# Kernel tuning notes

Measured on AMD Instinct MI355X. Metric: run time of the kernel, lower is better.

## Reference

```python
import jax, jax.numpy as jnp
import numpy as np

B, T, M_DIM, P_DIM = 32, 192, 256, 16
D, HE, HD, HG = 1024, 1024, 1024, 512
NH, DH, DFF, NL = 16, 64, 4096, 8
CTX = 10
E = P_DIM // 2  # num_experts = d_phase // 2
PRELU_A = 0.25  # torch PReLU default init slope (treated as constant)
LN_EPS = 1e-5


def prelu(x):
    return jnp.where(x >= 0, x, PRELU_A * x)


def layer_norm(x, g, b):
    m = x.mean(-1, keepdims=True)
    v = ((x - m) ** 2).mean(-1, keepdims=True)
    return (x - m) * jax.lax.rsqrt(v + LN_EPS) * g + b


def setup_inputs() -> dict:
    key = jax.random.key(0)
    ks = iter(jax.random.split(key, 64))
    w = lambda *s: jax.random.normal(next(ks), s, jnp.float32) * 0.02
    return dict(
        motion=jax.random.normal(next(ks), (B, T, M_DIM), jnp.float32),
        phase=jax.random.normal(next(ks), (B, T, P_DIM), jnp.float32),
        enc_W1=w(M_DIM + 1 + P_DIM, HE), enc_b1=w(HE), enc_W2=w(HE, D), enc_b2=w(D),
        kf_W1=w(2, D), kf_b1=w(D), kf_W2=w(D, D), kf_b2=w(D),
        rp_W1=w(1, DH), rp_b1=w(DH), rp_W2=w(DH, DH), rp_b2=w(DH),
        att_Wq=w(NL, D, NH * DH), att_bq=w(NL, NH * DH),
        att_Wk=w(NL, D, NH * DH), att_bk=w(NL, NH * DH),
        att_Wv=w(NL, D, NH * DH), att_bv=w(NL, NH * DH),
        att_Wo=w(NL, NH * DH, D), att_bo=w(NL, D),
        att_ln_g=jnp.ones((NL, D)), att_ln_b=jnp.zeros((NL, D)),
        pff_W1=w(NL, D, DFF), pff_b1=w(NL, DFF),
        pff_W2=w(NL, DFF, D), pff_b2=w(NL, D),
        pff_ln_g=jnp.ones((NL, D)), pff_ln_b=jnp.zeros((NL, D)),
        fin_ln_g=jnp.ones(D), fin_ln_b=jnp.zeros(D),
        pd_W1=w(D, HD), pd_b1=w(HD), pd_W2=w(HD, P_DIM), pd_b2=w(P_DIM),
        g_W1=w(P_DIM, HG), g_b1=w(HG), g_W2=w(HG, HG), g_b2=w(HG),
        g_W3=w(HG, E), g_b3=w(E),
        md_W0=w(E, D, HD), md_b0=w(E, HD),
        md_W1=w(E, HD, HD), md_b1=w(E, HD),
        md_W2=w(E, HD, M_DIM), md_b2=w(E, M_DIM),
    )


def reference(motion, phase, enc_W1, enc_b1, enc_W2, enc_b2,
              kf_W1, kf_b1, kf_W2, kf_b2, rp_W1, rp_b1, rp_W2, rp_b2,
              att_Wq, att_bq, att_Wk, att_bk, att_Wv, att_bv, att_Wo, att_bo,
              att_ln_g, att_ln_b, pff_W1, pff_b1, pff_W2, pff_b2, pff_ln_g, pff_ln_b,
              fin_ln_g, fin_ln_b, pd_W1, pd_b1, pd_W2, pd_b2,
              g_W1, g_b1, g_W2, g_b2, g_W3, g_b3,
              md_W0, md_b0, md_W1, md_b1, md_W2, md_b2):
    frames = jnp.arange(T)
    # eval mode: no midway targets; keyframes = context frames + last frame
    key_mask = (frames < CTX) | (frames == T - 1)          # [T]
    dm = key_mask.astype(motion.dtype)[:, None]            # data mask [T,1]
    x = jnp.concatenate([motion * dm,
                         jnp.broadcast_to(dm, (B, T, 1)),
                         phase * dm], axis=-1)
    x = prelu(x @ enc_W1 + enc_b1)
    x = prelu(x @ enc_W2 + enc_b2)                          # [B,T,D]
    # keyframe position embedding (distance to last context / target frame)
    ctx_idx = (frames - (CTX - 1)).astype(x.dtype)
    tgt_idx = -(frames - (T - 1)).astype(x.dtype)
    kp = jnp.stack([ctx_idx, tgt_idx], axis=-1)            # [T,2]
    x = x + (prelu(kp @ kf_W1 + kf_b1) @ kf_W2 + kf_b2)
    # relative position embedding, offsets -(T-1)..(T-1)
    rp = jnp.arange(-T + 1, T, dtype=x.dtype)[:, None]     # [2T-1,1]
    rel = prelu(rp @ rp_W1 + rp_b1) @ rp_W2 + rp_b2        # [2T-1,DH]
    rel_idx = frames[None, :] - frames[:, None] + (T - 1)  # [T,T] -> index into 2T-1
    blocked = ~key_mask                                    # attention mask: only attend to keyframes
    neg = jnp.asarray(-1e9, x.dtype)
    scale = 1.0 / np.sqrt(DH)

    def block(x, p):
        Wq, bq, Wk, bk, Wv, bv, Wo, bo, lg, lb, pW1, pb1, pW2, pb2, plg, plb = p
        h = layer_norm(x, lg, lb)                          # pre_lnorm
        q = (h @ Wq + bq).reshape(B, T, NH, DH)
        k = (h @ Wk + bk).reshape(B, T, NH, DH)
        v = (h @ Wv + bv).reshape(B, T, NH, DH)
        ac = jnp.einsum('bind,bjnd->bnij', q, k)           # content score
        bd = jnp.einsum('bind,rd->bnir', q, rel)           # rel-pos score (shared across heads' rel emb)
        bd = jnp.take_along_axis(bd, jnp.broadcast_to(rel_idx[None, None], ac.shape), axis=-1)
        s = (ac + bd) * scale
        s = jnp.where(blocked[None, None, None, :], neg, s)
        a = jax.nn.softmax(s, axis=-1)
        o = jnp.einsum('bnij,bjnd->bind', a, v).reshape(B, T, NH * DH)
        x = x + o @ Wo + bo
        h2 = layer_norm(x, plg, plb)
        x = x + jax.nn.relu(h2 @ pW1 + pb1) @ pW2 + pb2    # positionwise FF
        return x, None

    layer_params = (att_Wq, att_bq, att_Wk, att_bk, att_Wv, att_bv, att_Wo, att_bo,
                    att_ln_g, att_ln_b, pff_W1, pff_b1, pff_W2, pff_b2, pff_ln_g, pff_ln_b)
    x, _ = jax.lax.scan(block, x, layer_params)
    x = layer_norm(x, fin_ln_g, fin_ln_b)                  # final LN (pre_lnorm)
    # phase decoder
    phase_out = prelu(x @ pd_W1 + pd_b1) @ pd_W2 + pd_b2   # [B,T,P]
    # gating network -> per-frame soft expert weights
    h = prelu(phase_out @ g_W1 + g_b1)
    h = prelu(h @ g_W2 + g_b2)
    gate = jax.nn.softmax(h @ g_W3 + g_b3, axis=-1)        # [B,T,E]

    def mlin(y, W, b):
        # MultiLinear + per-frame expert blend: sum_e gate_e * (y @ W_e + b_e)
        return jnp.einsum('btd,edh,bte->bth', y, W, gate) + jnp.einsum('bte,eh->bth', gate, b)

    y = prelu(mlin(x, md_W0, md_b0))
    y = prelu(mlin(y, md_W1, md_b1))
    y = mlin(y, md_W2, md_b2)                              # [B,T,M]
    return y, phase_out
```

## Files before the change

### kernel.cpp

```cpp
#include <hip/hip_runtime.h>
#include <stdint.h>

typedef unsigned short u16;
typedef __attribute__((ext_vector_type(4))) float f32x4;
typedef __attribute__((ext_vector_type(8))) __bf16 bf16x8;

#define NT 6144
#define TT 192
#define PRELU_A 0.25f

__device__ __forceinline__ u16 f2bf(float f) {
  unsigned u = __float_as_uint(f);
  u += 0x7fffu + ((u >> 16) & 1u);
  return (u16)(u >> 16);
}
__device__ __forceinline__ float bf2f(u16 u) {
  return __uint_as_float(((unsigned)u) << 16);
}

__device__ __forceinline__ void gload16(const u16* g, __bf16* l) {
  auto* l3 = reinterpret_cast<__attribute__((address_space(3))) __bf16*>(
      reinterpret_cast<uintptr_t>(l));
  const auto* g1 = reinterpret_cast<const __attribute__((address_space(1))) u16*>(
      reinterpret_cast<uintptr_t>(g));
  __builtin_amdgcn_global_load_lds(g1, l3, 16, 0, 0);
}

__global__ __launch_bounds__(256)
void transpose_bf16(const float* __restrict__ src, u16* __restrict__ dst,
                    int K, int N, int Kp, int Np, long sstride, long dstride)
{
  src += (long)blockIdx.z * sstride;
  dst += (long)blockIdx.z * dstride;
  __shared__ float tile[64][65];
  const int kt = blockIdx.y * 64, nt = blockIdx.x * 64;
  #pragma unroll
  for (int i = 0; i < 16; ++i) {
    int idx = threadIdx.x + i*256;
    int kl = idx >> 6, nl = idx & 63;
    int k = kt + kl, n = nt + nl;
    tile[kl][nl] = (k < K && n < N) ? src[(long)k*N + n] : 0.f;
  }
  __syncthreads();
  #pragma unroll
  for (int i = 0; i < 16; ++i) {
    int idx = threadIdx.x + i*256;
    int nl = idx >> 6, kl = idx & 63;
    int n = nt + nl, k = kt + kl;
    if (n < Np && k < Kp) dst[(long)n*Kp + k] = f2bf(tile[kl][nl]);
  }
}

template<int MR, int HM>
__device__ __forceinline__ void epilogue_store(
    f32x4 (&acc)[MR][4], long arow0, long brow0, int wm, int wn, int lane,
    const float* bias, int biasN,
    float* Cf, int ldc, int Nf, int accum,
    u16* Cb, int ldcb, int Nb, int act)
{
  const int rbase = wm*HM + ((lane >> 4) << 2);
  const int cbase = wn*64 + (lane & 15);
  #pragma unroll
  for (int m = 0; m < MR; ++m) {
    #pragma unroll
    for (int n = 0; n < 4; ++n) {
      const long gcol = brow0 + cbase + n*16;
      const float bv = (bias && gcol < biasN) ? bias[gcol] : 0.f;
      #pragma unroll
      for (int r = 0; r < 4; ++r) {
        const long grow = arow0 + rbase + m*16 + r;
        float v = acc[m][n][r] + bv;
        if (act == 1) v = fmaxf(v, 0.f);
        else if (act == 2) v = (v >= 0.f) ? v : PRELU_A * v;
        if (Cf && gcol < Nf) {
          const long idx = grow * (long)ldc + gcol;
          Cf[idx] = accum ? (Cf[idx] + v) : v;
        }
        if (Cb && gcol < Nb) Cb[grow * (long)ldcb + gcol] = f2bf(v);
      }
    }
  }
}

__global__ __launch_bounds__(256, 3)
void gemm64(const u16* __restrict__ A, const u16* __restrict__ Bt,
            const float* __restrict__ bias, int biasN,
            float* __restrict__ Cf, int ldc, int Nf, int accum,
            u16* __restrict__ Cb, int ldcb, int Nb,
            int K, int act)
{
  __shared__ __bf16 As[2*64*64];
  __shared__ __bf16 Bs[2*128*64];
  const int tid = threadIdx.x;
  const int wid = tid >> 6;
  const int lane = tid & 63;
  const int wm = wid >> 1, wn = wid & 1;
  const long arow0 = (long)blockIdx.x * 64;
  const long brow0 = (long)blockIdx.y * 128;
  const int lr  = lane >> 3;
  const int lko = ((lane & 7) ^ (lane >> 3)) << 3;

  f32x4 acc[2][4];
  #pragma unroll
  for (int m = 0; m < 2; ++m)
    #pragma unroll
    for (int n = 0; n < 4; ++n) acc[m][n] = (f32x4)0.f;

  const int aro = lane & 15;
  const int g = lane >> 4;

  auto stage = [&](int buf, int kt) {
    #pragma unroll
    for (int c = wid; c < 24; c += 4) {
      if (c < 8) gload16(A + (arow0 + c*8 + lr)*K + kt + lko, As + buf*(64*64) + c*512);
      else       gload16(Bt + (brow0 + (c-8)*8 + lr)*K + kt + lko,
                         Bs + buf*(128*64) + (c-8)*512);
    }
  };

  const int nt = K >> 6;
  stage(0, 0);
  for (int t = 0; t < nt; ++t) {
    if (t + 1 < nt) {
      stage((t+1) & 1, (t+1) << 6);
      asm volatile("s_waitcnt vmcnt(6)" ::: "memory");
    } else {
      asm volatile("s_waitcnt vmcnt(0)" ::: "memory");
    }
    __builtin_amdgcn_s_barrier();
    __builtin_amdgcn_sched_barrier(0);
    const __bf16* Ab = As + (t&1)*(64*64);
    const __bf16* Bb = Bs + (t&1)*(128*64);
    #pragma unroll
    for (int kk = 0; kk < 2; ++kk) {
      bf16x8 af[2], bfv[4];
      #pragma unroll
      for (int m = 0; m < 2; ++m) {
        const int R = wm*32 + m*16 + aro;
        af[m] = *(const bf16x8*)(Ab + R*64 + (((kk*4 + g) ^ (R & 7)) << 3));
      }
      #pragma unroll
      for (int n = 0; n < 4; ++n) {
        const int R = wn*64 + n*16 + aro;
        bfv[n] = *(const bf16x8*)(Bb + R*64 + (((kk*4 + g) ^ (R & 7)) << 3));
      }
      #pragma unroll
      for (int m = 0; m < 2; ++m)
        #pragma unroll
        for (int n = 0; n < 4; ++n)
          acc[m][n] = __builtin_amdgcn_mfma_f32_16x16x32_bf16(af[m], bfv[n], acc[m][n], 0, 0, 0);
    }
    __builtin_amdgcn_sched_barrier(0);
    __builtin_amdgcn_s_barrier();
  }
  epilogue_store<2,32>(acc, arow0, brow0, wm, wn, lane,
                       bias, biasN, Cf, ldc, Nf, accum, Cb, ldcb, Nb, act);
}

__global__ __launch_bounds__(256, 3)
void gemm128(const u16* __restrict__ A, const u16* __restrict__ Bt,
             const float* __restrict__ bias, int biasN,
             float* __restrict__ Cf, int ldc, int Nf, int accum,
             u16* __restrict__ Cb, int ldcb, int Nb,
             int K, int act)
{
  __shared__ __bf16 As[3*128*32];
  __shared__ __bf16 Bs[3*128*32];
  const int tid = threadIdx.x;
  const int wid = tid >> 6;
  const int lane = tid & 63;
  const int wm = wid >> 1, wn = wid & 1;
  const long arow0 = (long)blockIdx.x * 128;
  const long brow0 = (long)blockIdx.y * 128;
  const int srow = lane >> 2;
  const int skoff = ((lane & 3) ^ ((lane >> 3) & 3)) << 3;

  f32x4 acc[4][4];
  #pragma unroll
  for (int m = 0; m < 4; ++m)
    #pragma unroll
    for (int n = 0; n < 4; ++n) acc[m][n] = (f32x4)0.f;

  const int aro = lane & 15;
  const int g = lane >> 4;

  auto stage = [&](int buf, int kt) {
    #pragma unroll
    for (int c = wid; c < 16; c += 4) {
      if (c < 8) gload16(A + (arow0 + c*16 + srow)*K + kt + skoff, As + buf*4096 + c*512);
      else       gload16(Bt + (brow0 + (c-8)*16 + srow)*K + kt + skoff,
                         Bs + buf*4096 + (c-8)*512);
    }
  };

  const int nt = K >> 5;
  stage(0, 0);
  if (nt > 1) stage(1, 32);

  int bcur = 0;
  for (int t = 0; t < nt; ++t) {
    if (t + 1 < nt) asm volatile("s_waitcnt vmcnt(4)" ::: "memory");
    else            asm volatile("s_waitcnt vmcnt(0)" ::: "memory");
    __builtin_amdgcn_s_barrier();
    __builtin_amdgcn_sched_barrier(0);
    if (t + 2 < nt) {
      int bnext = bcur + 2; if (bnext >= 3) bnext -= 3;
      stage(bnext, (t + 2) * 32);
    }
    const __bf16* Ab = As + bcur*4096;
    const __bf16* Bb = Bs + bcur*4096;
    bf16x8 af[4], bfv[4];
    #pragma unroll
    for (int m = 0; m < 4; ++m) {
      const int R = wm*64 + m*16 + aro;
      af[m] = *(const bf16x8*)(Ab + R*32 + ((g ^ ((R >> 1) & 3)) << 3));
    }
    #pragma unroll
    for (int n = 0; n < 4; ++n) {
      const int R = wn*64 + n*16 + aro;
      bfv[n] = *(const bf16x8*)(Bb + R*32 + ((g ^ ((R >> 1) & 3)) << 3));
    }
    #pragma unroll
    for (int m = 0; m < 4; ++m)
      #pragma unroll
      for (int n = 0; n < 4; ++n)
        acc[m][n] = __builtin_amdgcn_mfma_f32_16x16x32_bf16(af[m], bfv[n], acc[m][n], 0, 0, 0);
    __builtin_amdgcn_sched_barrier(0);
    bcur = (bcur + 1 == 3) ? 0 : bcur + 1;
  }
  epilogue_store<4,64>(acc, arow0, brow0, wm, wn, lane,
                       bias, biasN, Cf, ldc, Nf, accum, Cb, ldcb, Nb, act);
}

__global__ __launch_bounds__(256)
void moe_blend(const u16* __restrict__ C, const float* __restrict__ gate,
               int e0, int nE, int H, float* __restrict__ acc, int init,
               int act, u16* __restrict__ outb, float* __restrict__ outf)
{
  const int h4 = H >> 2;
  const long idx = (long)blockIdx.x*256 + threadIdx.x;
  if (idx >= (long)NT * h4) return;
  const long t = idx / h4;
  const int h = (int)(idx % h4) << 2;
  const long rowW = (long)nE * H;
  float4 s;
  if (init) { s.x = s.y = s.z = s.w = 0.f; }
  else s = ((const float4*)acc)[idx];
  for (int j = 0; j < nE; ++j) {
    const float gv = gate[t*8 + e0 + j];
    const ushort4 c4 = *(const ushort4*)(C + t*rowW + j*H + h);
    s.x += gv * bf2f(c4.x); s.y += gv * bf2f(c4.y);
    s.z += gv * bf2f(c4.z); s.w += gv * bf2f(c4.w);
  }
  const bool fin = (outb != nullptr) || (outf != nullptr);
  if (!fin) { ((float4*)acc)[idx] = s; return; }
  if (act == 2) {
    s.x = (s.x >= 0.f) ? s.x : PRELU_A * s.x;
    s.y = (s.y >= 0.f) ? s.y : PRELU_A * s.y;
    s.z = (s.z >= 0.f) ? s.z : PRELU_A * s.z;
    s.w = (s.w >= 0.f) ? s.w : PRELU_A * s.w;
  }
  if (outf) ((float4*)outf)[idx] = s;
  if (outb) {
    ushort4 o; o.x = f2bf(s.x); o.y = f2bf(s.y); o.z = f2bf(s.z); o.w = f2bf(s.w);
    *(ushort4*)(outb + t*(long)H + h) = o;
  }
}

__global__ __launch_bounds__(256)
void build_xin(const float* __restrict__ motion, const float* __restrict__ phase,
               u16* __restrict__ xin)
{
  const long idx = (long)blockIdx.x*256 + threadIdx.x;
  if (idx >= (long)NT*320) return;
  const int c = (int)(idx % 320);
  const long row = idx / 320;
  const int t = (int)(row % TT);
  const bool dm = (t < 10) || (t == TT-1);
  float v;
  if (c < 256)       v = dm ? motion[row*256 + c] : 0.f;
  else if (c == 256) v = dm ? 1.f : 0.f;
  else if (c < 273)  v = dm ? phase[row*16 + (c-257)] : 0.f;
  else               v = 0.f;
  xin[idx] = f2bf(v);
}

__global__ __launch_bounds__(256)
void build_kp(u16* __restrict__ kp)
{
  const int idx = blockIdx.x*256 + threadIdx.x;
  if (idx >= 256*64) return;
  const int r = idx / 64, c = idx % 64;
  float v = 0.f;
  if (r < TT) {
    if (c == 0) v = (float)(r - 9);
    else if (c == 1) v = (float)(TT-1 - r);
  }
  kp[idx] = f2bf(v);
}

__global__ __launch_bounds__(256)
void cat_kv_bias(const float* __restrict__ bk, const float* __restrict__ bv,
                 float* __restrict__ kvb)
{
  const int idx = blockIdx.x*256 + threadIdx.x;
  if (idx >= 8*2048) return;
  const int l = idx >> 11, c = idx & 2047;
  kvb[idx] = (c < 1024) ? bk[l*1024 + c] : bv[l*1024 + c - 1024];
}

__global__ __launch_bounds__(64)
void relpos(const float* __restrict__ W1, const float* __restrict__ b1,
            const float* __restrict__ W2, const float* __restrict__ b2,
            float* __restrict__ rel)
{
  const int r = blockIdx.x;
  const int d = threadIdx.x;
  __shared__ float h[64];
  const float rp = (float)(r - (TT-1));
  float hv = rp * W1[d] + b1[d];
  hv = (hv >= 0.f) ? hv : PRELU_A * hv;
  h[d] = hv;
  __syncthreads();
  if (r < 2*TT - 1) {
    float o = b2[d];
    for (int j = 0; j < 64; ++j) o += h[j] * W2[j*64 + d];
    rel[r*64 + d] = o;
  } else {
    rel[r*64 + d] = 0.f;
  }
}

__global__ __launch_bounds__(256)
void ln_bf16(const float* __restrict__ x, const float* __restrict__ g,
             const float* __restrict__ b, u16* __restrict__ out)
{
  const long row = blockIdx.x;
  const float4 v = ((const float4*)(x + row*1024))[threadIdx.x];
  float s  = v.x + v.y + v.z + v.w;
  float s2 = v.x*v.x + v.y*v.y + v.z*v.z + v.w*v.w;
  #pragma unroll
  for (int m = 32; m; m >>= 1) { s += __shfl_xor(s, m); s2 += __shfl_xor(s2, m); }
  __shared__ float red[8];
  const int wid = threadIdx.x >> 6;
  if ((threadIdx.x & 63) == 0) { red[wid] = s; red[wid+4] = s2; }
  __syncthreads();
  s  = red[0] + red[1] + red[2] + red[3];
  s2 = red[4] + red[5] + red[6] + red[7];
  const float mean = s * (1.f/1024.f);
  const float var  = fmaxf(s2 * (1.f/1024.f) - mean*mean, 0.f);
  const float rs   = rsqrtf(var + 1e-5f);
  const float4 gg = ((const float4*)g)[threadIdx.x];
  const float4 bb = ((const float4*)b)[threadIdx.x];
  ushort4 o;
  o.x = f2bf((v.x-mean)*rs*gg.x + bb.x);
  o.y = f2bf((v.y-mean)*rs*gg.y + bb.y);
  o.z = f2bf((v.z-mean)*rs*gg.z + bb.z);
  o.w = f2bf((v.w-mean)*rs*gg.w + bb.w);
  ((ushort4*)(out + row*1024))[threadIdx.x] = o;
}

__global__ __launch_bounds__(128)
void gather_hk(const u16* __restrict__ h, u16* __restrict__ hk)
{
  const int r = blockIdx.x;
  uint4 val;
  if (r < 352) {
    const int b = r / 11, j = r - b*11;
    const int fr = (j < 10) ? j : (TT-1);
    val = ((const uint4*)(h + (long)(b*TT + fr)*1024))[threadIdx.x];
  } else { val.x = val.y = val.z = val.w = 0u; }
  ((uint4*)(hk + (long)r*1024))[threadIdx.x] = val;
}

__global__ __launch_bounds__(256)
void attn11(const float* __restrict__ q, const float* __restrict__ kv,
            const float* __restrict__ rel, u16* __restrict__ o)
{
  const int w = (blockIdx.x << 2) + (threadIdx.x >> 6);
  const int lane = threadIdx.x & 63;
  const int n = w & 15;
  const int row = w >> 4;
  const int b = row / TT, i = row - b*TT;
  const float qd = q[(long)row*1024 + n*64 + lane];
  float s[11];
  #pragma unroll
  for (int j = 0; j < 11; ++j) {
    const int kf = (j < 10) ? j : (TT-1);
    float t = qd * (kv[(long)(b*11 + j)*2048 + n*64 + lane]
                    + rel[(kf - i + TT-1)*64 + lane]);
    #pragma unroll
    for (int m = 32; m; m >>= 1) t += __shfl_xor(t, m);
    s[j] = t * 0.125f;
  }
  float mx = s[0];
  #pragma unroll
  for (int j = 1; j < 11; ++j) mx = fmaxf(mx, s[j]);
  float den = 0.f, e[11];
  #pragma unroll
  for (int j = 0; j < 11; ++j) { e[j] = __expf(s[j] - mx); den += e[j]; }
  const float inv = 1.f / den;
  float od = 0.f;
  #pragma unroll
  for (int j = 0; j < 11; ++j)
    od += e[j] * kv[(long)(b*11 + j)*2048 + 1024 + n*64 + lane];
  o[(long)row*1024 + n*64 + lane] = f2bf(od * inv);
}

__global__ __launch_bounds__(256)
void kfadd(float* __restrict__ x, const float* __restrict__ kfe)
{
  const long idx = (long)blockIdx.x*256 + threadIdx.x;
  if (idx >= (long)NT*256) return;
  const int t = (int)((idx >> 8) % TT);
  const int c4 = (int)(idx & 255);
  float4 a = ((float4*)x)[idx];
  const float4 kk = ((const float4*)kfe)[t*256 + c4];
  a.x += kk.x; a.y += kk.y; a.z += kk.z; a.w += kk.w;
  ((float4*)x)[idx] = a;
}

__global__ __launch_bounds__(256)
void softmax8(const float* __restrict__ lg, float* __restrict__ gate)
{
  const int t = blockIdx.x*256 + threadIdx.x;
  if (t >= NT) return;
  float v[8], mx = -1e30f;
  #pragma unroll
  for (int e = 0; e < 8; ++e) { v[e] = lg[t*8 + e]; mx = fmaxf(mx, v[e]); }
  float den = 0.f;
  #pragma unroll
  for (int e = 0; e < 8; ++e) { v[e] = __expf(v[e] - mx); den += v[e]; }
  const float inv = 1.f / den;
  #pragma unroll
  for (int e = 0; e < 8; ++e) gate[t*8 + e] = v[e] * inv;
}

extern "C" void kernel_launch(void* const* d_in, const int* in_sizes, int n_in,
                              void* d_out, int out_size, void* d_ws, size_t ws_size,
                              hipStream_t stream)
{
  (void)in_sizes; (void)n_in; (void)out_size; (void)ws_size;
  const float* motion  = (const float*)d_in[0];
  const float* phase   = (const float*)d_in[1];
  const float* enc_W1  = (const float*)d_in[2];
  const float* enc_b1  = (const float*)d_in[3];
  const float* enc_W2  = (const float*)d_in[4];
  const float* enc_b2  = (const float*)d_in[5];
  const float* kf_W1   = (const float*)d_in[6];
  const float* kf_b1   = (const float*)d_in[7];
  const float* kf_W2   = (const float*)d_in[8];
  const float* kf_b2   = (const float*)d_in[9];
  const float* rp_W1   = (const float*)d_in[10];
  const float* rp_b1   = (const float*)d_in[11];
  const float* rp_W2   = (const float*)d_in[12];
  const float* rp_b2   = (const float*)d_in[13];
  const float* att_Wq  = (const float*)d_in[14];
  const float* att_bq  = (const float*)d_in[15];
  const float* att_Wk  = (const float*)d_in[16];
  const float* att_bk  = (const float*)d_in[17];
  const float* att_Wv  = (const float*)d_in[18];
  const float* att_bv  = (const float*)d_in[19];
  const float* att_Wo  = (const float*)d_in[20];
  const float* att_bo  = (const float*)d_in[21];
  const float* att_ln_g = (const float*)d_in[22];
  const float* att_ln_b = (const float*)d_in[23];
  const float* pff_W1  = (const float*)d_in[24];
  const float* pff_b1  = (const float*)d_in[25];
  const float* pff_W2  = (const float*)d_in[26];
  const float* pff_b2  = (const float*)d_in[27];
  const float* pff_ln_g = (const float*)d_in[28];
  const float* pff_ln_b = (const float*)d_in[29];
  const float* fin_ln_g = (const float*)d_in[30];
  const float* fin_ln_b = (const float*)d_in[31];
  const float* pd_W1   = (const float*)d_in[32];
  const float* pd_b1   = (const float*)d_in[33];
  const float* pd_W2   = (const float*)d_in[34];
  const float* pd_b2   = (const float*)d_in[35];
  const float* g_W1    = (const float*)d_in[36];
  const float* g_b1    = (const float*)d_in[37];
  const float* g_W2    = (const float*)d_in[38];
  const float* g_b2    = (const float*)d_in[39];
  const float* g_W3    = (const float*)d_in[40];
  const float* g_b3    = (const float*)d_in[41];
  const float* md_W0   = (const float*)d_in[42];
  const float* md_b0   = (const float*)d_in[43];
  const float* md_W1   = (const float*)d_in[44];
  const float* md_b1   = (const float*)d_in[45];
  const float* md_W2   = (const float*)d_in[46];
  const float* md_b2   = (const float*)d_in[47];

  char* wsp = (char*)d_ws;
  size_t off = 0;
  auto alloc = [&](size_t bytes) -> char* {
    char* p = wsp + off;
    off += (bytes + 255) & ~(size_t)255;
    return p;
  };

  u16* encW1T = (u16*)alloc((size_t)1024*320*2);
  u16* encW2T = (u16*)alloc((size_t)1024*1024*2);
  u16* kfW1T  = (u16*)alloc((size_t)1024*64*2);
  u16* kfW2T  = (u16*)alloc((size_t)1024*1024*2);
  u16* WqT    = (u16*)alloc((size_t)8*1024*1024*2);
  u16* kvT    = (u16*)alloc((size_t)8*2048*1024*2);
  u16* WoT    = (u16*)alloc((size_t)8*1024*1024*2);
  u16* F1T    = (u16*)alloc((size_t)8*4096*1024*2);
  u16* F2T    = (u16*)alloc((size_t)8*1024*4096*2);
  u16* pdW1T  = (u16*)alloc((size_t)1024*1024*2);
  u16* pdW2T  = (u16*)alloc((size_t)128*1024*2);
  u16* gW1T   = (u16*)alloc((size_t)512*64*2);
  u16* gW2T   = (u16*)alloc((size_t)512*512*2);
  u16* gW3T   = (u16*)alloc((size_t)128*512*2);
  u16* md0T   = (u16*)alloc((size_t)8*1024*1024*2);
  u16* md1T   = (u16*)alloc((size_t)8*1024*1024*2);
  u16* md2T   = (u16*)alloc((size_t)8*256*1024*2);

  float* x    = (float*)alloc((size_t)NT*1024*4);
  float* rel  = (float*)alloc((size_t)384*64*4);
  u16*   kp   = (u16*)  alloc((size_t)256*64*2);
  u16*   kf1  = (u16*)  alloc((size_t)256*1024*2);
  float* kfe  = (float*)alloc((size_t)256*1024*4);
  u16*   hk   = (u16*)  alloc((size_t)384*1024*2);
  float* kvb  = (float*)alloc((size_t)8*2048*4);
  float* kvbuf= (float*)alloc((size_t)384*2048*4);
  u16*   phbf = (u16*)  alloc((size_t)NT*64*2);
  float* glog = (float*)alloc((size_t)NT*8*4);
  float* gate = (float*)alloc((size_t)NT*8*4);
  u16*   xin  = (u16*)  alloc((size_t)NT*320*2);
  u16*   s1   = (u16*)  alloc((size_t)NT*1024*2);
  float* s2   = (float*)alloc((size_t)NT*1024*4);
  u16*   s3   = (u16*)  alloc((size_t)NT*1024*2);
  char*  s4c  =         alloc((size_t)NT*4096*2);
  u16*   s4   = (u16*)s4c;

  float* outY = (float*)d_out;
  float* outP = outY + (size_t)NT*256;

  auto tr = [&](const float* s_, u16* d_, int K, int N, int Kp, int Np, int batch,
                long dstride) {
    dim3 g((Np+63)/64, (Kp+63)/64, batch);
    transpose_bf16<<<g, 256, 0, stream>>>(s_, d_, K, N, Kp, Np, (long)K*N, dstride);
  };
  auto g64 = [&](const u16* A, const u16* Bt, const float* bias, int biasN,
                 float* Cf, int ldc, int Nf, int accum,
                 u16* Cb, int ldcb, int Nb, int M, int K, int Npad, int act) {
    gemm64<<<dim3(M/64, Npad/128), 256, 0, stream>>>(
        A, Bt, bias, biasN, Cf, ldc, Nf, accum, Cb, ldcb, Nb, K, act);
  };
  auto g128 = [&](const u16* A, const u16* Bt, const float* bias, int biasN,
                  float* Cf, int ldc, int Nf, int accum,
                  u16* Cb, int ldcb, int Nb, int M, int K, int Npad, int act) {
    gemm128<<<dim3(M/128, Npad/128), 256, 0, stream>>>(
        A, Bt, bias, biasN, Cf, ldc, Nf, accum, Cb, ldcb, Nb, K, act);
  };

  tr(enc_W1, encW1T, 273, 1024, 320, 1024, 1, (long)1024*320);
  tr(enc_W2, encW2T, 1024, 1024, 1024, 1024, 1, (long)1024*1024);
  tr(kf_W1,  kfW1T,  2, 1024, 64, 1024, 1, (long)1024*64);
  tr(kf_W2,  kfW2T,  1024, 1024, 1024, 1024, 1, (long)1024*1024);
  tr(att_Wq, WqT, 1024, 1024, 1024, 1024, 8, (long)1024*1024);
  tr(att_Wk, kvT,               1024, 1024, 1024, 1024, 8, (long)2048*1024);
  tr(att_Wv, kvT + (size_t)1024*1024, 1024, 1024, 1024, 1024, 8, (long)2048*1024);
  tr(att_Wo, WoT, 1024, 1024, 1024, 1024, 8, (long)1024*1024);
  tr(pff_W1, F1T, 1024, 4096, 1024, 4096, 8, (long)4096*1024);
  tr(pff_W2, F2T, 4096, 1024, 4096, 1024, 8, (long)1024*4096);
  tr(pd_W1,  pdW1T, 1024, 1024, 1024, 1024, 1, (long)1024*1024);
  tr(pd_W2,  pdW2T, 1024, 16, 1024, 128, 1, (long)128*1024);
  tr(g_W1,   gW1T, 16, 512, 64, 512, 1, (long)512*64);
  tr(g_W2,   gW2T, 512, 512, 512, 512, 1, (long)512*512);
  tr(g_W3,   gW3T, 512, 8, 512, 128, 1, (long)128*512);
  tr(md_W0,  md0T, 1024, 1024, 1024, 1024, 8, (long)1024*1024);
  tr(md_W1,  md1T, 1024, 1024, 1024, 1024, 8, (long)1024*1024);
  tr(md_W2,  md2T, 1024, 256, 1024, 256, 8, (long)256*1024);

  build_xin<<<(NT*320 + 255)/256, 256, 0, stream>>>(motion, phase, xin);
  build_kp<<<(256*64 + 255)/256, 256, 0, stream>>>(kp);
  cat_kv_bias<<<(8*2048 + 255)/256, 256, 0, stream>>>(att_bk, att_bv, kvb);
  relpos<<<384, 64, 0, stream>>>(rp_W1, rp_b1, rp_W2, rp_b2, rel);

  g64(xin, encW1T, enc_b1, 1024, nullptr,0,0,0, s1,1024,1024, NT, 320, 1024, 2);
  g64(s1,  encW2T, enc_b2, 1024, x,1024,1024,0, nullptr,0,0, NT, 1024, 1024, 2);
  g64(kp,  kfW1T, kf_b1, 1024, nullptr,0,0,0, kf1,1024,1024, 256, 64, 1024, 2);
  g64(kf1, kfW2T, kf_b2, 1024, kfe,1024,1024,0, nullptr,0,0, 256, 1024, 1024, 0);
  kfadd<<<NT, 256, 0, stream>>>(x, kfe);

  for (int l = 0; l < 8; ++l) {
    const size_t w1 = (size_t)l*1024*1024;
    const size_t wf = (size_t)l*4096*1024;
    ln_bf16<<<NT, 256, 0, stream>>>(x, att_ln_g + l*1024, att_ln_b + l*1024, s1);
    gather_hk<<<384, 128, 0, stream>>>(s1, hk);
    g64(s1, WqT + w1, att_bq + l*1024, 1024, s2,1024,1024,0, nullptr,0,0, NT, 1024, 1024, 0);
    g64(hk, kvT + (size_t)l*2048*1024, kvb + l*2048, 2048,
        kvbuf,2048,2048,0, nullptr,0,0, 384, 1024, 2048, 0);
    attn11<<<(NT*16)/4, 256, 0, stream>>>(s2, kvbuf, rel, s3);
    g64(s3, WoT + w1, att_bo + l*1024, 1024, x,1024,1024,1, nullptr,0,0, NT, 1024, 1024, 0);
    ln_bf16<<<NT, 256, 0, stream>>>(x, pff_ln_g + l*1024, pff_ln_b + l*1024, s1);
    g128(s1, F1T + wf, pff_b1 + l*4096, 4096, nullptr,0,0,0, s4,4096,4096, NT, 1024, 4096, 1);
    g64(s4, F2T + wf, pff_b2 + l*1024, 1024, x,1024,1024,1, nullptr,0,0, NT, 4096, 1024, 0);
  }

  ln_bf16<<<NT, 256, 0, stream>>>(x, fin_ln_g, fin_ln_b, s1);
  g64(s1, pdW1T, pd_b1, 1024, nullptr,0,0,0, s3,1024,1024, NT, 1024, 1024, 2);
  g64(s3, pdW2T, pd_b2, 16, outP,16,16,0, phbf,64,64, NT, 1024, 128, 0);

  g64(phbf, gW1T, g_b1, 512, nullptr,0,0,0, s3,512,512, NT, 64, 512, 2);
  g64(s3,   gW2T, g_b2, 512, nullptr,0,0,0, s4,512,512, NT, 512, 512, 2);
  g64(s4,   gW3T, g_b3, 8,  glog,8,8,0, nullptr,0,0, NT, 512, 128, 0);
  softmax8<<<(NT + 255)/256, 256, 0, stream>>>(glog, gate);

  const int BL = (NT*1024/4 + 255)/256;
  g128(s1, md0T,             md_b0,        4096, nullptr,0,0,0, s4,4096,4096, NT, 1024, 4096, 0);
  moe_blend<<<BL, 256, 0, stream>>>(s4, gate, 0, 4, 1024, s2, 1, 0, nullptr, nullptr);
  g128(s1, md0T + (size_t)4096*1024, md_b0 + 4096, 4096, nullptr,0,0,0, s4,4096,4096, NT, 1024, 4096, 0);
  moe_blend<<<BL, 256, 0, stream>>>(s4, gate, 4, 4, 1024, s2, 0, 2, s3, nullptr);
  g128(s3, md1T,             md_b1,        4096, nullptr,0,0,0, s4,4096,4096, NT, 1024, 4096, 0);
  moe_blend<<<BL, 256, 0, stream>>>(s4, gate, 0, 4, 1024, s2, 1, 0, nullptr, nullptr);
  g128(s3, md1T + (size_t)4096*1024, md_b1 + 4096, 4096, nullptr,0,0,0, s4,4096,4096, NT, 1024, 4096, 0);
  moe_blend<<<BL, 256, 0, stream>>>(s4, gate, 4, 4, 1024, s2, 0, 2, s1, nullptr);
  g128(s1, md2T, md_b2, 2048, nullptr,0,0,0, s4,2048,2048, NT, 1024, 2048, 0);
  moe_blend<<<(NT*256/4 + 255)/256, 256, 0, stream>>>(s4, gate, 0, 8, 256, nullptr, 1, 0, nullptr, outY);
}
```

Before: 3.465 ms.

## Remap GEMM blocks across XCDs, fuse key gather into LN, rewrite attention

Adds an XCD-aware workgroup remap to both GEMM kernels so that consecutive tiles land on the same XCD, aiming to improve L2 reuse. Folds the key-frame gather into the layernorm kernel, removing one launch per layer. Rewrites the 11-key attention so each thread handles a whole (row, head) with float4 loads instead of per-lane shuffle reductions. The new attention has less parallelism and strided access, and the hk padding rows are no longer zeroed each layer.

```diff
diff --git a/kernel.cpp b/kernel.cpp
--- a/kernel.cpp
+++ b/kernel.cpp
@@ -24,6 +24,17 @@
   const auto* g1 = reinterpret_cast<const __attribute__((address_space(1))) u16*>(
       reinterpret_cast<uintptr_t>(g));
   __builtin_amdgcn_global_load_lds(g1, l3, 16, 0, 0);
+}
+
+__device__ __forceinline__ void xcd_remap(int& bx, int& by)
+{
+  const int nwg = gridDim.x * gridDim.y;
+  const int f = blockIdx.y * gridDim.x + blockIdx.x;
+  const int q = nwg >> 3, r = nwg & 7;
+  const int xcd = f & 7, s = f >> 3;
+  const int w = (xcd < r ? xcd*(q+1) : r*(q+1) + (xcd-r)*q) + s;
+  by = w % gridDim.y;
+  bx = w / gridDim.y;
 }
 
 __global__ __launch_bounds__(256)
@@ -95,8 +106,9 @@
   const int wid = tid >> 6;
   const int lane = tid & 63;
   const int wm = wid >> 1, wn = wid & 1;
-  const long arow0 = (long)blockIdx.x * 64;
-  const long brow0 = (long)blockIdx.y * 128;
+  int bx, by; xcd_remap(bx, by);
+  const long arow0 = (long)bx * 64;
+  const long brow0 = (long)by * 128;
   const int lr  = lane >> 3;
   const int lko = ((lane & 7) ^ (lane >> 3)) << 3;
 
@@ -170,8 +182,9 @@
   const int wid = tid >> 6;
   const int lane = tid & 63;
   const int wm = wid >> 1, wn = wid & 1;
-  const long arow0 = (long)blockIdx.x * 128;
-  const long brow0 = (long)blockIdx.y * 128;
+  int bx, by; xcd_remap(bx, by);
+  const long arow0 = (long)bx * 128;
+  const long brow0 = (long)by * 128;
   const int srow = lane >> 2;
   const int skoff = ((lane & 3) ^ ((lane >> 3) & 3)) << 3;
 
@@ -333,7 +346,8 @@
 
 __global__ __launch_bounds__(256)
 void ln_bf16(const float* __restrict__ x, const float* __restrict__ g,
-             const float* __restrict__ b, u16* __restrict__ out)
+             const float* __restrict__ b, u16* __restrict__ out,
+             u16* __restrict__ hk)
 {
   const long row = blockIdx.x;
   const float4 v = ((const float4*)(x + row*1024))[threadIdx.x];
@@ -358,53 +372,64 @@
   o.z = f2bf((v.z-mean)*rs*gg.z + bb.z);
   o.w = f2bf((v.w-mean)*rs*gg.w + bb.w);
   ((ushort4*)(out + row*1024))[threadIdx.x] = o;
-}
-
-__global__ __launch_bounds__(128)
-void gather_hk(const u16* __restrict__ h, u16* __restrict__ hk)
-{
-  const int r = blockIdx.x;
-  uint4 val;
-  if (r < 352) {
-    const int b = r / 11, j = r - b*11;
-    const int fr = (j < 10) ? j : (TT-1);
-    val = ((const uint4*)(h + (long)(b*TT + fr)*1024))[threadIdx.x];
-  } else { val.x = val.y = val.z = val.w = 0u; }
-  ((uint4*)(hk + (long)r*1024))[threadIdx.x] = val;
+  if (hk) {
+    const int t = (int)(row % TT);
+    if (t < 10 || t == TT-1) {
+      const int bidx = (int)(row / TT);
+      const int j = (t < 10) ? t : 10;
+      ((ushort4*)(hk + (long)(bidx*11 + j)*1024))[threadIdx.x] = o;
+    }
+  }
 }
 
 __global__ __launch_bounds__(256)
 void attn11(const float* __restrict__ q, const float* __restrict__ kv,
             const float* __restrict__ rel, u16* __restrict__ o)
 {
-  const int w = (blockIdx.x << 2) + (threadIdx.x >> 6);
-  const int lane = threadIdx.x & 63;
-  const int n = w & 15;
-  const int row = w >> 4;
+  const int idx = blockIdx.x*256 + threadIdx.x;
+  const int n = idx & 15;
+  const int row = idx >> 4;
   const int b = row / TT, i = row - b*TT;
-  const float qd = q[(long)row*1024 + n*64 + lane];
+  const float4* qp = (const float4*)(q + (long)row*1024 + n*64);
+  float4 qv[16];
+  #pragma unroll
+  for (int d = 0; d < 16; ++d) qv[d] = qp[d];
   float s[11];
   #pragma unroll
   for (int j = 0; j < 11; ++j) {
     const int kf = (j < 10) ? j : (TT-1);
-    float t = qd * (kv[(long)(b*11 + j)*2048 + n*64 + lane]
-                    + rel[(kf - i + TT-1)*64 + lane]);
-    #pragma unroll
-    for (int m = 32; m; m >>= 1) t += __shfl_xor(t, m);
-    s[j] = t * 0.125f;
+    const float4* kp = (const float4*)(kv + (long)(b*11 + j)*2048 + n*64);
+    const float4* rp = (const float4*)(rel + (kf - i + TT-1)*64);
+    float acc = 0.f;
+    #pragma unroll
+    for (int d = 0; d < 16; ++d) {
+      const float4 k4 = kp[d], r4 = rp[d];
+      acc += qv[d].x*(k4.x+r4.x) + qv[d].y*(k4.y+r4.y)
+           + qv[d].z*(k4.z+r4.z) + qv[d].w*(k4.w+r4.w);
+    }
+    s[j] = acc * 0.125f;
   }
   float mx = s[0];
   #pragma unroll
   for (int j = 1; j < 11; ++j) mx = fmaxf(mx, s[j]);
-  float den = 0.f, e[11];
+  float e[11], den = 0.f;
   #pragma unroll
   for (int j = 0; j < 11; ++j) { e[j] = __expf(s[j] - mx); den += e[j]; }
   const float inv = 1.f / den;
-  float od = 0.f;
-  #pragma unroll
-  for (int j = 0; j < 11; ++j)
-    od += e[j] * kv[(long)(b*11 + j)*2048 + 1024 + n*64 + lane];
-  o[(long)row*1024 + n*64 + lane] = f2bf(od * inv);
+  #pragma unroll
+  for (int j = 0; j < 11; ++j) e[j] *= inv;
+  u16* op = o + (long)row*1024 + n*64;
+  #pragma unroll
+  for (int d = 0; d < 16; ++d) {
+    float ax = 0.f, ay = 0.f, az = 0.f, aw = 0.f;
+    #pragma unroll
+    for (int j = 0; j < 11; ++j) {
+      const float4 v4 = *(const float4*)(kv + (long)(b*11 + j)*2048 + 1024 + n*64 + d*4);
+      ax += e[j]*v4.x; ay += e[j]*v4.y; az += e[j]*v4.z; aw += e[j]*v4.w;
+    }
+    ushort4 ov; ov.x = f2bf(ax); ov.y = f2bf(ay); ov.z = f2bf(az); ov.w = f2bf(aw);
+    ((ushort4*)op)[d] = ov;
+  }
 }
 
 __global__ __launch_bounds__(256)
@@ -588,19 +613,18 @@
   for (int l = 0; l < 8; ++l) {
     const size_t w1 = (size_t)l*1024*1024;
     const size_t wf = (size_t)l*4096*1024;
-    ln_bf16<<<NT, 256, 0, stream>>>(x, att_ln_g + l*1024, att_ln_b + l*1024, s1);
-    gather_hk<<<384, 128, 0, stream>>>(s1, hk);
+    ln_bf16<<<NT, 256, 0, stream>>>(x, att_ln_g + l*1024, att_ln_b + l*1024, s1, hk);
     g64(s1, WqT + w1, att_bq + l*1024, 1024, s2,1024,1024,0, nullptr,0,0, NT, 1024, 1024, 0);
     g64(hk, kvT + (size_t)l*2048*1024, kvb + l*2048, 2048,
         kvbuf,2048,2048,0, nullptr,0,0, 384, 1024, 2048, 0);
-    attn11<<<(NT*16)/4, 256, 0, stream>>>(s2, kvbuf, rel, s3);
+    attn11<<<NT*16/256, 256, 0, stream>>>(s2, kvbuf, rel, s3);
     g64(s3, WoT + w1, att_bo + l*1024, 1024, x,1024,1024,1, nullptr,0,0, NT, 1024, 1024, 0);
-    ln_bf16<<<NT, 256, 0, stream>>>(x, pff_ln_g + l*1024, pff_ln_b + l*1024, s1);
+    ln_bf16<<<NT, 256, 0, stream>>>(x, pff_ln_g + l*1024, pff_ln_b + l*1024, s1, nullptr);
     g128(s1, F1T + wf, pff_b1 + l*4096, 4096, nullptr,0,0,0, s4,4096,4096, NT, 1024, 4096, 1);
     g64(s4, F2T + wf, pff_b2 + l*1024, 1024, x,1024,1024,1, nullptr,0,0, NT, 4096, 1024, 0);
   }
 
-  ln_bf16<<<NT, 256, 0, stream>>>(x, fin_ln_g, fin_ln_b, s1);
+  ln_bf16<<<NT, 256, 0, stream>>>(x, fin_ln_g, fin_ln_b, s1, nullptr);
   g64(s1, pdW1T, pd_b1, 1024, nullptr,0,0,0, s3,1024,1024, NT, 1024, 1024, 2);
   g64(s3, pdW2T, pd_b2, 16, outP,16,16,0, phbf,64,64, NT, 1024, 128, 0);
 
```

Result: slower. 3.614 ms (+4.3%).
